# Kernel optimization log

Measured on AMD Instinct MI355X. Metric: run time of the kernel, lower is better.

## Reference

```python
import jax, jax.numpy as jnp
import numpy as np

RBF_DIM = 16
RBF_DMAX = 10.0
EPS = 1e-8


def _rbf(d):
    # GVP-style radial basis featurization: [..., RBF_DIM]
    mu = jnp.linspace(0.0, RBF_DMAX, RBF_DIM)
    sigma = RBF_DMAX / RBF_DIM
    return jnp.exp(-(((d[..., None] - mu) / sigma) ** 2))


def _norm_no_nan(x):
    return jnp.sqrt(jnp.clip(jnp.sum(x * x, axis=-1), EPS, None))


def setup_inputs() -> dict:
    key = jax.random.key(0)
    ks = jax.random.split(key, 16)
    N, Eu = 100000, 800000
    D_node, D_edge = 128, 64
    n_a, n_e = 16, 5
    s_t = jax.random.normal(ks[0], (N, D_node), jnp.float32)
    x_t = jax.random.normal(ks[1], (N, 3), jnp.float32) * 3.0
    v_t = jax.random.normal(ks[2], (N, 4, 3), jnp.float32)
    e_t = jax.random.normal(ks[3], (2 * Eu, D_edge), jnp.float32)
    dst_lig_x = x_t + jax.random.normal(ks[4], (N, 3), jnp.float32)
    dst_lig_a = jax.random.uniform(ks[5], (N, n_a), jnp.float32)
    dst_lig_e = jax.random.uniform(ks[6], (Eu, n_e), jnp.float32)
    # symmetric edge list: first Eu edges are "upper", second Eu their mirror
    src_u = jax.random.randint(ks[7], (Eu,), 0, N)
    dst_u = jax.random.randint(ks[8], (Eu,), 0, N)
    edge_src = jnp.concatenate([src_u, dst_u]).astype(jnp.int64)
    edge_dst = jnp.concatenate([dst_u, src_u]).astype(jnp.int64)
    # node residual MLP params (in = rbf + one-hot lig_a + s_t)
    din_n = RBF_DIM + n_a + D_node
    W1 = jax.random.normal(ks[9], (din_n, D_node), jnp.float32) / np.sqrt(din_n)
    b1 = jnp.zeros((D_node,), jnp.float32)
    W2 = jax.random.normal(ks[10], (D_node, D_node), jnp.float32) / np.sqrt(D_node)
    b2 = jnp.zeros((D_node,), jnp.float32)
    # edge residual MLP params (in = e_t + lig_e pred + rbf)
    din_e = D_edge + n_e + RBF_DIM
    We = jax.random.normal(ks[11], (din_e, D_edge), jnp.float32) / np.sqrt(din_e)
    be = jnp.zeros((D_edge,), jnp.float32)
    return {"s_t": s_t, "x_t": x_t, "v_t": v_t, "e_t": e_t,
            "dst_lig_x": dst_lig_x, "dst_lig_a": dst_lig_a, "dst_lig_e": dst_lig_e,
            "edge_src": edge_src, "edge_dst": edge_dst,
            "W1": W1, "b1": b1, "W2": W2, "b2": b2, "We": We, "be": be}


def reference(s_t, x_t, v_t, e_t, dst_lig_x, dst_lig_a, dst_lig_e,
              edge_src, edge_dst, W1, b1, W2, b2, We, be):
    # ---- node residual (lig_x generated -> RBF of |x_pred - x_t|; lig_a generated -> pred) ----
    x_diff = dst_lig_x - x_t                      # [N,3]
    dij = _norm_no_nan(x_diff)                    # [N]
    node_in = jnp.concatenate([_rbf(dij), dst_lig_a, s_t], axis=-1)
    h = jax.nn.silu(node_in @ W1 + b1)
    node_res = jax.nn.silu(h @ W2 + b2)
    node_out = s_t + node_res
    # overwrite last vector channel with unit displacement
    v_out = v_t.at[:, -1, :].set(x_diff / dij[:, None])
    # ---- lig_to_lig edge residual on upper edges, mirrored to lower edges ----
    Eu = edge_src.shape[0] // 2
    su, du = edge_src[:Eu], edge_dst[:Eu]
    d_t = _norm_no_nan(x_t[su] - x_t[du])         # current distances
    d_1 = _norm_no_nan(dst_lig_x[su] - dst_lig_x[du])  # predicted distances
    d_input = _rbf(d_1) - _rbf(d_t)               # [Eu, RBF_DIM]
    e_u = e_t[:Eu]
    edge_in = jnp.concatenate([e_u, dst_lig_e, d_input], axis=-1)
    edge_res = jax.nn.silu(edge_in @ We + be)
    feats = e_u + edge_res
    # original scatters feats into both upper-mask and ~upper-mask slots
    e_out = jnp.concatenate([feats, feats], axis=0)
    return node_out, v_out, e_out
```

## Files before the change

### kernel.cpp

```cpp
#include <hip/hip_runtime.h>
#include <math.h>

typedef short bf16x8 __attribute__((ext_vector_type(8)));
typedef float f32x4 __attribute__((ext_vector_type(4)));
typedef float fvec4 __attribute__((ext_vector_type(4)));

#define EBK 128

__device__ __forceinline__ float silu_f(float x) {
  return x / (1.0f + __expf(-x));
}
__device__ __forceinline__ unsigned short f2bf(float x) {
  union { float f; unsigned u; } v; v.f = x;
  unsigned r = v.u + 0x7FFFu + ((v.u >> 16) & 1u);
  return (unsigned short)(r >> 16);
}
__device__ __forceinline__ float bf2f(unsigned short h) {
  union { unsigned u; float f; } v; v.u = ((unsigned)h) << 16; return v.f;
}

__global__ __launch_bounds__(256)
void prep_kernel(const float* __restrict__ W1, const float* __restrict__ W2,
                 const float* __restrict__ We, unsigned short* __restrict__ ws)
{
  int i = blockIdx.x * 256 + threadIdx.x;
  if (i < 6144) {
    int col = i / 96, k = i - col * 96;
    float v = (k < 85) ? We[k * 64 + col] : 0.0f;
    ws[i] = f2bf(v);
  }
  int j = i - 6144;
  if (j >= 0 && j < 20480) {
    int col = j / 160, k = j - col * 160;
    ws[6144 + j] = f2bf(W1[k * 128 + col]);
  }
  int l = i - 26624;
  if (l >= 0 && l < 16384) {
    int col = l >> 7, k = l & 127;
    ws[26624 + l] = f2bf(W2[k * 128 + col]);
  }
}

__global__ __launch_bounds__(256, 4)
void node_kernel(const float* __restrict__ s_t,
                 const float* __restrict__ x_t,
                 const float* __restrict__ v_t,
                 const float* __restrict__ dst_lig_x,
                 const float* __restrict__ dst_lig_a,
                 const unsigned short* __restrict__ w1t, const float* __restrict__ b1,
                 const unsigned short* __restrict__ w2t, const float* __restrict__ b2,
                 float* __restrict__ node_out, float* __restrict__ v_out,
                 int N)
{
  __shared__ unsigned short A1[64][168];
  __shared__ unsigned short H [64][136];
  const int t = threadIdx.x;
  const int row0 = blockIdx.x * 64;
  const int w = t >> 6, lane = t & 63;

  #pragma unroll
  for (int p = 0; p < 8; ++p) {
    int i = p * 256 + t;
    int row = i >> 5, q = i & 31;
    if (row0 + row < N) {
      const fvec4 v = __builtin_nontemporal_load(
          reinterpret_cast<const fvec4*>(&s_t[(size_t)(row0 + row) * 128 + q * 4]));
      uint2 pk;
      pk.x = f2bf(v.x) | ((unsigned)f2bf(v.y) << 16);
      pk.y = f2bf(v.z) | ((unsigned)f2bf(v.w) << 16);
      *reinterpret_cast<uint2*>(&A1[row][32 + q * 4]) = pk;
    }
  }
  #pragma unroll
  for (int p = 0; p < 4; ++p) {
    int i = p * 256 + t;
    int el = i >> 4, m = i & 15;
    int row = row0 + el;
    if (row < N) {
      float dx = dst_lig_x[row*3+0] - x_t[row*3+0];
      float dy = dst_lig_x[row*3+1] - x_t[row*3+1];
      float dz = dst_lig_x[row*3+2] - x_t[row*3+2];
      float dij = sqrtf(fmaxf(dx*dx + dy*dy + dz*dz, 1e-8f));
      float tt = (dij - 0.66666667f * (float)m) * 1.6f;
      A1[el][m]      = f2bf(__expf(-tt * tt));
      A1[el][16 + m] = f2bf(dst_lig_a[(size_t)row * 16 + m]);
      if (m < 12) {
        float val;
        if (m < 9)       val = v_t[(size_t)row * 12 + m];
        else if (m == 9) val = dx / dij;
        else if (m == 10)val = dy / dij;
        else             val = dz / dij;
        __builtin_nontemporal_store(val, &v_out[(size_t)row * 12 + m]);
      }
    }
  }
  __syncthreads();

  const int mb = (w & 1) * 32;
  const int nb = (w >> 1) * 64;

  f32x4 acc[2][4] = {};
  #pragma unroll 1
  for (int ks = 0; ks < 5; ++ks) {
    const int ko = ks * 32 + ((lane >> 4) << 3);
    bf16x8 af[2], bfr[4];
    #pragma unroll
    for (int m = 0; m < 2; ++m)
      af[m] = *reinterpret_cast<const bf16x8*>(&A1[mb + m*16 + (lane & 15)][ko]);
    #pragma unroll
    for (int n = 0; n < 4; ++n)
      bfr[n] = *reinterpret_cast<const bf16x8*>(&w1t[(size_t)(nb + n*16 + (lane & 15)) * 160 + ko]);
    #pragma unroll
    for (int m = 0; m < 2; ++m)
      #pragma unroll
      for (int n = 0; n < 4; ++n)
        acc[m][n] = __builtin_amdgcn_mfma_f32_16x16x32_bf16(af[m], bfr[n], acc[m][n], 0, 0, 0);
  }
  #pragma unroll
  for (int n = 0; n < 4; ++n) {
    float bb = b1[nb + n*16 + (lane & 15)];
    #pragma unroll
    for (int m = 0; m < 2; ++m) {
      int r0 = mb + m*16 + ((lane >> 4) << 2);
      int c  = nb + n*16 + (lane & 15);
      #pragma unroll
      for (int r = 0; r < 4; ++r)
        H[r0 + r][c] = f2bf(silu_f(acc[m][n][r] + bb));
    }
  }
  __syncthreads();

  f32x4 acc2[2][4] = {};
  #pragma unroll 1
  for (int ks = 0; ks < 4; ++ks) {
    const int ko = ks * 32 + ((lane >> 4) << 3);
    bf16x8 af[2], bfr[4];
    #pragma unroll
    for (int m = 0; m < 2; ++m)
      af[m] = *reinterpret_cast<const bf16x8*>(&H[mb + m*16 + (lane & 15)][ko]);
    #pragma unroll
    for (int n = 0; n < 4; ++n)
      bfr[n] = *reinterpret_cast<const bf16x8*>(&w2t[(size_t)(nb + n*16 + (lane & 15)) * 128 + ko]);
    #pragma unroll
    for (int m = 0; m < 2; ++m)
      #pragma unroll
      for (int n = 0; n < 4; ++n)
        acc2[m][n] = __builtin_amdgcn_mfma_f32_16x16x32_bf16(af[m], bfr[n], acc2[m][n], 0, 0, 0);
  }
  #pragma unroll
  for (int n = 0; n < 4; ++n) {
    float bb = b2[nb + n*16 + (lane & 15)];
    #pragma unroll
    for (int m = 0; m < 2; ++m) {
      int r0 = mb + m*16 + ((lane >> 4) << 2);
      int c  = nb + n*16 + (lane & 15);
      #pragma unroll
      for (int r = 0; r < 4; ++r) {
        int row = row0 + r0 + r;
        if (row < N) {
          float o = bf2f(A1[r0 + r][32 + c]) + silu_f(acc2[m][n][r] + bb);
          __builtin_nontemporal_store(o, &node_out[(size_t)row * 128 + c]);
        }
      }
    }
  }
}

__global__ __launch_bounds__(256, 4)
void edge_kernel(const float* __restrict__ e_t,
                 const float* __restrict__ x_t,
                 const float* __restrict__ dst_lig_x,
                 const float* __restrict__ dst_lig_e,
                 const int* __restrict__ edge_src,
                 const int* __restrict__ edge_dst,
                 const unsigned short* __restrict__ wet, const float* __restrict__ be,
                 float* __restrict__ e_out0, float* __restrict__ e_out1,
                 int Eu)
{
  __shared__ unsigned short A[EBK][104];
  const int t = threadIdx.x;
  const int e0 = blockIdx.x * EBK;
  const int w = t >> 6, lane = t & 63;

  #pragma unroll
  for (int p = 0; p < 8; ++p) {
    int i = p * 256 + t;
    int row = i >> 4, cq = i & 15;
    if (e0 + row < Eu) {
      const fvec4 v = __builtin_nontemporal_load(
          reinterpret_cast<const fvec4*>(&e_t[(size_t)(e0 + row) * 64 + cq * 4]));
      uint2 pk;
      pk.x = f2bf(v.x) | ((unsigned)f2bf(v.y) << 16);
      pk.y = f2bf(v.z) | ((unsigned)f2bf(v.w) << 16);
      *reinterpret_cast<uint2*>(&A[row][cq * 4]) = pk;
    }
  }
  {
    const int el = t >> 1, which = t & 1;
    const int e = e0 + el;
    float dcur = 0.0f;
    if (e < Eu) {
      int su = edge_src[e], du = edge_dst[e];
      const float* base = which ? dst_lig_x : x_t;
      float u0 = base[su*3+0] - base[du*3+0];
      float u1 = base[su*3+1] - base[du*3+1];
      float u2 = base[su*3+2] - base[du*3+2];
      dcur = sqrtf(fmaxf(u0*u0 + u1*u1 + u2*u2, 1e-8f));
    }
    float doth = __shfl_xor(dcur, 1);
    float dt_ = which ? doth : dcur;
    float d1_ = which ? dcur : doth;
    if (e < Eu) {
      #pragma unroll
      for (int q = 0; q < 8; ++q) {
        int m = which * 8 + q;
        float mu = 0.66666667f * (float)m;
        float a1 = (d1_ - mu) * 1.6f, a2 = (dt_ - mu) * 1.6f;
        A[el][69 + m] = f2bf(__expf(-a1*a1) - __expf(-a2*a2));
      }
    }
  }
  #pragma unroll
  for (int q = 0; q < 3; ++q) {
    int i = q * 256 + t;
    if (i < EBK * 5) {
      int el = i / 5, c = i - el * 5;
      if (e0 + el < Eu) A[el][64 + c] = f2bf(dst_lig_e[(size_t)(e0 + el) * 5 + c]);
    }
  }
  #pragma unroll
  for (int q = 0; q < 6; ++q) {
    int i = q * 256 + t;
    if (i < EBK * 11) { int el = i / 11, c = i - el * 11; A[el][85 + c] = 0; }
  }
  __syncthreads();

  const int mb = w * 32;

  f32x4 acc[2][4] = {};
  #pragma unroll 1
  for (int ks = 0; ks < 3; ++ks) {
    const int ko = ks * 32 + ((lane >> 4) << 3);
    bf16x8 af[2], bfr[4];
    #pragma unroll
    for (int m = 0; m < 2; ++m)
      af[m] = *reinterpret_cast<const bf16x8*>(&A[mb + m*16 + (lane & 15)][ko]);
    #pragma unroll
    for (int n = 0; n < 4; ++n)
      bfr[n] = *reinterpret_cast<const bf16x8*>(&wet[(size_t)(n*16 + (lane & 15)) * 96 + ko]);
    #pragma unroll
    for (int m = 0; m < 2; ++m)
      #pragma unroll
      for (int n = 0; n < 4; ++n)
        acc[m][n] = __builtin_amdgcn_mfma_f32_16x16x32_bf16(af[m], bfr[n], acc[m][n], 0, 0, 0);
  }
  #pragma unroll
  for (int n = 0; n < 4; ++n) {
    float bb = be[n*16 + (lane & 15)];
    #pragma unroll
    for (int m = 0; m < 2; ++m) {
      int r0 = mb + m*16 + ((lane >> 4) << 2);
      int c  = n*16 + (lane & 15);
      #pragma unroll
      for (int r = 0; r < 4; ++r) {
        size_t eidx = (size_t)e0 + r0 + r;
        if ((int)eidx < Eu) {
          float feat = bf2f(A[r0 + r][c]) + silu_f(acc[m][n][r] + bb);
          __builtin_nontemporal_store(feat, &e_out0[eidx * 64 + c]);
          __builtin_nontemporal_store(feat, &e_out1[eidx * 64 + c]);
        }
      }
    }
  }
}

extern "C" void kernel_launch(void* const* d_in, const int* in_sizes, int n_in,
                              void* d_out, int out_size, void* d_ws, size_t ws_size,
                              hipStream_t stream) {
  const float* s_t       = (const float*)d_in[0];
  const float* x_t       = (const float*)d_in[1];
  const float* v_t       = (const float*)d_in[2];
  const float* e_t       = (const float*)d_in[3];
  const float* dst_lig_x = (const float*)d_in[4];
  const float* dst_lig_a = (const float*)d_in[5];
  const float* dst_lig_e = (const float*)d_in[6];
  const int*   edge_src  = (const int*)d_in[7];
  const int*   edge_dst  = (const int*)d_in[8];
  const float* W1        = (const float*)d_in[9];
  const float* b1        = (const float*)d_in[10];
  const float* W2        = (const float*)d_in[11];
  const float* b2        = (const float*)d_in[12];
  const float* We        = (const float*)d_in[13];
  const float* be        = (const float*)d_in[14];

  const int N  = in_sizes[0] / 128;
  const int Eu = in_sizes[3] / 128;

  float* out      = (float*)d_out;
  float* node_out = out;
  float* v_out    = out + (size_t)N * 128;
  float* e_out0   = v_out + (size_t)N * 12;
  float* e_out1   = e_out0 + (size_t)Eu * 64;

  unsigned short* wsp = (unsigned short*)d_ws;
  unsigned short* wet = wsp;
  unsigned short* w1t = wsp + 6144;
  unsigned short* w2t = wsp + 26624;

  prep_kernel<<<168, 256, 0, stream>>>(W1, W2, We, wsp);

  edge_kernel<<<(Eu + EBK - 1) / EBK, 256, 0, stream>>>(
      e_t, x_t, dst_lig_x, dst_lig_e, edge_src, edge_dst, wet, be,
      e_out0, e_out1, Eu);

  node_kernel<<<(N + 63) / 64, 256, 0, stream>>>(
      s_t, x_t, v_t, dst_lig_x, dst_lig_a, w1t, b1, w2t, b2,
      node_out, v_out, N);
}
```

Before: 255.7 us.

## Fuse node and edge kernels into one launch with interleaved block roles

Merges the separate edge and node kernels into a single kernel. Every fifth block does node work and the other blocks do edge work, with shared memory held in a union. This removes one launch and the tail bubble between the two kernels, and lets node and edge blocks run on the GPU at the same time. In exchange the shared memory per block becomes the larger of the two layouts and register use is the maximum of both paths, which could lower occupancy for edge blocks.

```diff
diff --git a/kernel.cpp b/kernel.cpp
--- a/kernel.cpp
+++ b/kernel.cpp
@@ -6,6 +6,7 @@
 typedef float fvec4 __attribute__((ext_vector_type(4)));
 
 #define EBK 128
+#define NBK 64
 
 __device__ __forceinline__ float silu_f(float x) {
   return x / (1.0f + __expf(-x));
@@ -41,233 +42,241 @@
   }
 }
 
+struct EdgeSmem { unsigned short A[EBK][104]; };
+struct NodeSmem { unsigned short A1[NBK][168]; unsigned short H[NBK][136]; };
+union FusedSmem { EdgeSmem e; NodeSmem n; };
+
 __global__ __launch_bounds__(256, 4)
-void node_kernel(const float* __restrict__ s_t,
-                 const float* __restrict__ x_t,
-                 const float* __restrict__ v_t,
-                 const float* __restrict__ dst_lig_x,
-                 const float* __restrict__ dst_lig_a,
-                 const unsigned short* __restrict__ w1t, const float* __restrict__ b1,
-                 const unsigned short* __restrict__ w2t, const float* __restrict__ b2,
-                 float* __restrict__ node_out, float* __restrict__ v_out,
-                 int N)
+void fused_kernel(const float* __restrict__ s_t,
+                  const float* __restrict__ x_t,
+                  const float* __restrict__ v_t,
+                  const float* __restrict__ e_t,
+                  const float* __restrict__ dst_lig_x,
+                  const float* __restrict__ dst_lig_a,
+                  const float* __restrict__ dst_lig_e,
+                  const int* __restrict__ edge_src,
+                  const int* __restrict__ edge_dst,
+                  const unsigned short* __restrict__ wsw,
+                  const float* __restrict__ b1, const float* __restrict__ b2,
+                  const float* __restrict__ be,
+                  float* __restrict__ node_out, float* __restrict__ v_out,
+                  float* __restrict__ e_out0, float* __restrict__ e_out1,
+                  int N, int Eu, int nNodeBlk, int nEdgeBlk)
 {
-  __shared__ unsigned short A1[64][168];
-  __shared__ unsigned short H [64][136];
+  __shared__ FusedSmem sm;
+  const int bid = blockIdx.x;
   const int t = threadIdx.x;
-  const int row0 = blockIdx.x * 64;
   const int w = t >> 6, lane = t & 63;
 
-  #pragma unroll
-  for (int p = 0; p < 8; ++p) {
-    int i = p * 256 + t;
-    int row = i >> 5, q = i & 31;
-    if (row0 + row < N) {
-      const fvec4 v = __builtin_nontemporal_load(
-          reinterpret_cast<const fvec4*>(&s_t[(size_t)(row0 + row) * 128 + q * 4]));
-      uint2 pk;
-      pk.x = f2bf(v.x) | ((unsigned)f2bf(v.y) << 16);
-      pk.y = f2bf(v.z) | ((unsigned)f2bf(v.w) << 16);
-      *reinterpret_cast<uint2*>(&A1[row][32 + q * 4]) = pk;
-    }
-  }
-  #pragma unroll
-  for (int p = 0; p < 4; ++p) {
-    int i = p * 256 + t;
-    int el = i >> 4, m = i & 15;
-    int row = row0 + el;
-    if (row < N) {
-      float dx = dst_lig_x[row*3+0] - x_t[row*3+0];
-      float dy = dst_lig_x[row*3+1] - x_t[row*3+1];
-      float dz = dst_lig_x[row*3+2] - x_t[row*3+2];
-      float dij = sqrtf(fmaxf(dx*dx + dy*dy + dz*dz, 1e-8f));
-      float tt = (dij - 0.66666667f * (float)m) * 1.6f;
-      A1[el][m]      = f2bf(__expf(-tt * tt));
-      A1[el][16 + m] = f2bf(dst_lig_a[(size_t)row * 16 + m]);
-      if (m < 12) {
-        float val;
-        if (m < 9)       val = v_t[(size_t)row * 12 + m];
-        else if (m == 9) val = dx / dij;
-        else if (m == 10)val = dy / dij;
-        else             val = dz / dij;
-        __builtin_nontemporal_store(val, &v_out[(size_t)row * 12 + m]);
-      }
-    }
-  }
-  __syncthreads();
-
-  const int mb = (w & 1) * 32;
-  const int nb = (w >> 1) * 64;
-
-  f32x4 acc[2][4] = {};
-  #pragma unroll 1
-  for (int ks = 0; ks < 5; ++ks) {
-    const int ko = ks * 32 + ((lane >> 4) << 3);
-    bf16x8 af[2], bfr[4];
-    #pragma unroll
-    for (int m = 0; m < 2; ++m)
-      af[m] = *reinterpret_cast<const bf16x8*>(&A1[mb + m*16 + (lane & 15)][ko]);
-    #pragma unroll
-    for (int n = 0; n < 4; ++n)
-      bfr[n] = *reinterpret_cast<const bf16x8*>(&w1t[(size_t)(nb + n*16 + (lane & 15)) * 160 + ko]);
-    #pragma unroll
-    for (int m = 0; m < 2; ++m)
+  if (bid % 5 == 4) {
+    const int nb = bid / 5;
+    if (nb >= nNodeBlk) return;
+    const int row0 = nb * NBK;
+    const unsigned short* w1t = wsw + 6144;
+    const unsigned short* w2t = wsw + 26624;
+    auto& A1 = sm.n.A1;
+    auto& H  = sm.n.H;
+
+    #pragma unroll
+    for (int p = 0; p < 8; ++p) {
+      int i = p * 256 + t;
+      int row = i >> 5, q = i & 31;
+      if (row0 + row < N) {
+        const fvec4 v = __builtin_nontemporal_load(
+            reinterpret_cast<const fvec4*>(&s_t[(size_t)(row0 + row) * 128 + q * 4]));
+        uint2 pk;
+        pk.x = f2bf(v.x) | ((unsigned)f2bf(v.y) << 16);
+        pk.y = f2bf(v.z) | ((unsigned)f2bf(v.w) << 16);
+        *reinterpret_cast<uint2*>(&A1[row][32 + q * 4]) = pk;
+      }
+    }
+    #pragma unroll
+    for (int p = 0; p < 4; ++p) {
+      int i = p * 256 + t;
+      int el = i >> 4, m = i & 15;
+      int row = row0 + el;
+      if (row < N) {
+        float dx = dst_lig_x[row*3+0] - x_t[row*3+0];
+        float dy = dst_lig_x[row*3+1] - x_t[row*3+1];
+        float dz = dst_lig_x[row*3+2] - x_t[row*3+2];
+        float dij = sqrtf(fmaxf(dx*dx + dy*dy + dz*dz, 1e-8f));
+        float tt = (dij - 0.66666667f * (float)m) * 1.6f;
+        A1[el][m]      = f2bf(__expf(-tt * tt));
+        A1[el][16 + m] = f2bf(dst_lig_a[(size_t)row * 16 + m]);
+        if (m < 12) {
+          float val;
+          if (m < 9)       val = v_t[(size_t)row * 12 + m];
+          else if (m == 9) val = dx / dij;
+          else if (m == 10)val = dy / dij;
+          else             val = dz / dij;
+          __builtin_nontemporal_store(val, &v_out[(size_t)row * 12 + m]);
+        }
+      }
+    }
+    __syncthreads();
+
+    const int mb = (w & 1) * 32;
+    const int nb2 = (w >> 1) * 64;
+
+    f32x4 acc[2][4] = {};
+    #pragma unroll 1
+    for (int ks = 0; ks < 5; ++ks) {
+      const int ko = ks * 32 + ((lane >> 4) << 3);
+      bf16x8 af[2], bfr[4];
+      #pragma unroll
+      for (int m = 0; m < 2; ++m)
+        af[m] = *reinterpret_cast<const bf16x8*>(&A1[mb + m*16 + (lane & 15)][ko]);
       #pragma unroll
       for (int n = 0; n < 4; ++n)
-        acc[m][n] = __builtin_amdgcn_mfma_f32_16x16x32_bf16(af[m], bfr[n], acc[m][n], 0, 0, 0);
-  }
-  #pragma unroll
-  for (int n = 0; n < 4; ++n) {
-    float bb = b1[nb + n*16 + (lane & 15)];
-    #pragma unroll
-    for (int m = 0; m < 2; ++m) {
-      int r0 = mb + m*16 + ((lane >> 4) << 2);
-      int c  = nb + n*16 + (lane & 15);
-      #pragma unroll
-      for (int r = 0; r < 4; ++r)
-        H[r0 + r][c] = f2bf(silu_f(acc[m][n][r] + bb));
-    }
-  }
-  __syncthreads();
-
-  f32x4 acc2[2][4] = {};
-  #pragma unroll 1
-  for (int ks = 0; ks < 4; ++ks) {
-    const int ko = ks * 32 + ((lane >> 4) << 3);
-    bf16x8 af[2], bfr[4];
-    #pragma unroll
-    for (int m = 0; m < 2; ++m)
-      af[m] = *reinterpret_cast<const bf16x8*>(&H[mb + m*16 + (lane & 15)][ko]);
-    #pragma unroll
-    for (int n = 0; n < 4; ++n)
-      bfr[n] = *reinterpret_cast<const bf16x8*>(&w2t[(size_t)(nb + n*16 + (lane & 15)) * 128 + ko]);
-    #pragma unroll
-    for (int m = 0; m < 2; ++m)
+        bfr[n] = *reinterpret_cast<const bf16x8*>(&w1t[(size_t)(nb2 + n*16 + (lane & 15)) * 160 + ko]);
+      #pragma unroll
+      for (int m = 0; m < 2; ++m)
+        #pragma unroll
+        for (int n = 0; n < 4; ++n)
+          acc[m][n] = __builtin_amdgcn_mfma_f32_16x16x32_bf16(af[m], bfr[n], acc[m][n], 0, 0, 0);
+    }
+    #pragma unroll
+    for (int n = 0; n < 4; ++n) {
+      float bb = b1[nb2 + n*16 + (lane & 15)];
+      #pragma unroll
+      for (int m = 0; m < 2; ++m) {
+        int r0 = mb + m*16 + ((lane >> 4) << 2);
+        int c  = nb2 + n*16 + (lane & 15);
+        #pragma unroll
+        for (int r = 0; r < 4; ++r)
+          H[r0 + r][c] = f2bf(silu_f(acc[m][n][r] + bb));
+      }
+    }
+    __syncthreads();
+
+    f32x4 acc2[2][4] = {};
+    #pragma unroll 1
+    for (int ks = 0; ks < 4; ++ks) {
+      const int ko = ks * 32 + ((lane >> 4) << 3);
+      bf16x8 af[2], bfr[4];
+      #pragma unroll
+      for (int m = 0; m < 2; ++m)
+        af[m] = *reinterpret_cast<const bf16x8*>(&H[mb + m*16 + (lane & 15)][ko]);
       #pragma unroll
       for (int n = 0; n < 4; ++n)
-        acc2[m][n] = __builtin_amdgcn_mfma_f32_16x16x32_bf16(af[m], bfr[n], acc2[m][n], 0, 0, 0);
-  }
-  #pragma unroll
-  for (int n = 0; n < 4; ++n) {
-    float bb = b2[nb + n*16 + (lane & 15)];
-    #pragma unroll
-    for (int m = 0; m < 2; ++m) {
-      int r0 = mb + m*16 + ((lane >> 4) << 2);
-      int c  = nb + n*16 + (lane & 15);
-      #pragma unroll
-      for (int r = 0; r < 4; ++r) {
-        int row = row0 + r0 + r;
-        if (row < N) {
-          float o = bf2f(A1[r0 + r][32 + c]) + silu_f(acc2[m][n][r] + bb);
-          __builtin_nontemporal_store(o, &node_out[(size_t)row * 128 + c]);
+        bfr[n] = *reinterpret_cast<const bf16x8*>(&w2t[(size_t)(nb2 + n*16 + (lane & 15)) * 128 + ko]);
+      #pragma unroll
+      for (int m = 0; m < 2; ++m)
+        #pragma unroll
+        for (int n = 0; n < 4; ++n)
+          acc2[m][n] = __builtin_amdgcn_mfma_f32_16x16x32_bf16(af[m], bfr[n], acc2[m][n], 0, 0, 0);
+    }
+    #pragma unroll
+    for (int n = 0; n < 4; ++n) {
+      float bb = b2[nb2 + n*16 + (lane & 15)];
+      #pragma unroll
+      for (int m = 0; m < 2; ++m) {
+        int r0 = mb + m*16 + ((lane >> 4) << 2);
+        int c  = nb2 + n*16 + (lane & 15);
+        #pragma unroll
+        for (int r = 0; r < 4; ++r) {
+          int row = row0 + r0 + r;
+          if (row < N) {
+            float o = bf2f(A1[r0 + r][32 + c]) + silu_f(acc2[m][n][r] + bb);
+            __builtin_nontemporal_store(o, &node_out[(size_t)row * 128 + c]);
+          }
         }
       }
     }
-  }
-}
-
-__global__ __launch_bounds__(256, 4)
-void edge_kernel(const float* __restrict__ e_t,
-                 const float* __restrict__ x_t,
-                 const float* __restrict__ dst_lig_x,
-                 const float* __restrict__ dst_lig_e,
-                 const int* __restrict__ edge_src,
-                 const int* __restrict__ edge_dst,
-                 const unsigned short* __restrict__ wet, const float* __restrict__ be,
-                 float* __restrict__ e_out0, float* __restrict__ e_out1,
-                 int Eu)
-{
-  __shared__ unsigned short A[EBK][104];
-  const int t = threadIdx.x;
-  const int e0 = blockIdx.x * EBK;
-  const int w = t >> 6, lane = t & 63;
-
-  #pragma unroll
-  for (int p = 0; p < 8; ++p) {
-    int i = p * 256 + t;
-    int row = i >> 4, cq = i & 15;
-    if (e0 + row < Eu) {
-      const fvec4 v = __builtin_nontemporal_load(
-          reinterpret_cast<const fvec4*>(&e_t[(size_t)(e0 + row) * 64 + cq * 4]));
-      uint2 pk;
-      pk.x = f2bf(v.x) | ((unsigned)f2bf(v.y) << 16);
-      pk.y = f2bf(v.z) | ((unsigned)f2bf(v.w) << 16);
-      *reinterpret_cast<uint2*>(&A[row][cq * 4]) = pk;
-    }
-  }
-  {
-    const int el = t >> 1, which = t & 1;
-    const int e = e0 + el;
-    float dcur = 0.0f;
-    if (e < Eu) {
-      int su = edge_src[e], du = edge_dst[e];
-      const float* base = which ? dst_lig_x : x_t;
-      float u0 = base[su*3+0] - base[du*3+0];
-      float u1 = base[su*3+1] - base[du*3+1];
-      float u2 = base[su*3+2] - base[du*3+2];
-      dcur = sqrtf(fmaxf(u0*u0 + u1*u1 + u2*u2, 1e-8f));
-    }
-    float doth = __shfl_xor(dcur, 1);
-    float dt_ = which ? doth : dcur;
-    float d1_ = which ? dcur : doth;
-    if (e < Eu) {
-      #pragma unroll
-      for (int q = 0; q < 8; ++q) {
-        int m = which * 8 + q;
-        float mu = 0.66666667f * (float)m;
-        float a1 = (d1_ - mu) * 1.6f, a2 = (dt_ - mu) * 1.6f;
-        A[el][69 + m] = f2bf(__expf(-a1*a1) - __expf(-a2*a2));
-      }
-    }
-  }
-  #pragma unroll
-  for (int q = 0; q < 3; ++q) {
-    int i = q * 256 + t;
-    if (i < EBK * 5) {
-      int el = i / 5, c = i - el * 5;
-      if (e0 + el < Eu) A[el][64 + c] = f2bf(dst_lig_e[(size_t)(e0 + el) * 5 + c]);
-    }
-  }
-  #pragma unroll
-  for (int q = 0; q < 6; ++q) {
-    int i = q * 256 + t;
-    if (i < EBK * 11) { int el = i / 11, c = i - el * 11; A[el][85 + c] = 0; }
-  }
-  __syncthreads();
-
-  const int mb = w * 32;
-
-  f32x4 acc[2][4] = {};
-  #pragma unroll 1
-  for (int ks = 0; ks < 3; ++ks) {
-    const int ko = ks * 32 + ((lane >> 4) << 3);
-    bf16x8 af[2], bfr[4];
-    #pragma unroll
-    for (int m = 0; m < 2; ++m)
-      af[m] = *reinterpret_cast<const bf16x8*>(&A[mb + m*16 + (lane & 15)][ko]);
-    #pragma unroll
-    for (int n = 0; n < 4; ++n)
-      bfr[n] = *reinterpret_cast<const bf16x8*>(&wet[(size_t)(n*16 + (lane & 15)) * 96 + ko]);
-    #pragma unroll
-    for (int m = 0; m < 2; ++m)
+  } else {
+    const int eb = bid - (bid + 1) / 5;
+    if (eb >= nEdgeBlk) return;
+    const int e0 = eb * EBK;
+    const unsigned short* wet = wsw;
+    auto& A = sm.e.A;
+
+    #pragma unroll
+    for (int p = 0; p < 8; ++p) {
+      int i = p * 256 + t;
+      int row = i >> 4, cq = i & 15;
+      if (e0 + row < Eu) {
+        const fvec4 v = __builtin_nontemporal_load(
+            reinterpret_cast<const fvec4*>(&e_t[(size_t)(e0 + row) * 64 + cq * 4]));
+        uint2 pk;
+        pk.x = f2bf(v.x) | ((unsigned)f2bf(v.y) << 16);
+        pk.y = f2bf(v.z) | ((unsigned)f2bf(v.w) << 16);
+        *reinterpret_cast<uint2*>(&A[row][cq * 4]) = pk;
+      }
+    }
+    {
+      const int el = t >> 1, which = t & 1;
+      const int e = e0 + el;
+      float dcur = 0.0f;
+      if (e < Eu) {
+        int su = edge_src[e], du = edge_dst[e];
+        const float* base = which ? dst_lig_x : x_t;
+        float u0 = base[su*3+0] - base[du*3+0];
+        float u1 = base[su*3+1] - base[du*3+1];
+        float u2 = base[su*3+2] - base[du*3+2];
+        dcur = sqrtf(fmaxf(u0*u0 + u1*u1 + u2*u2, 1e-8f));
+      }
+      float doth = __shfl_xor(dcur, 1);
+      float dt_ = which ? doth : dcur;
+      float d1_ = which ? dcur : doth;
+      if (e < Eu) {
+        #pragma unroll
+        for (int q = 0; q < 8; ++q) {
+          int m = which * 8 + q;
+          float mu = 0.66666667f * (float)m;
+          float a1 = (d1_ - mu) * 1.6f, a2 = (dt_ - mu) * 1.6f;
+          A[el][69 + m] = f2bf(__expf(-a1*a1) - __expf(-a2*a2));
+        }
+      }
+    }
+    #pragma unroll
+    for (int q = 0; q < 3; ++q) {
+      int i = q * 256 + t;
+      if (i < EBK * 5) {
+        int el = i / 5, c = i - el * 5;
+        if (e0 + el < Eu) A[el][64 + c] = f2bf(dst_lig_e[(size_t)(e0 + el) * 5 + c]);
+      }
+    }
+    #pragma unroll
+    for (int q = 0; q < 6; ++q) {
+      int i = q * 256 + t;
+      if (i < EBK * 11) { int el = i / 11, c = i - el * 11; A[el][85 + c] = 0; }
+    }
+    __syncthreads();
+
+    const int mb = w * 32;
+
+    f32x4 acc[2][4] = {};
+    #pragma unroll 1
+    for (int ks = 0; ks < 3; ++ks) {
+      const int ko = ks * 32 + ((lane >> 4) << 3);
+      bf16x8 af[2], bfr[4];
+      #pragma unroll
+      for (int m = 0; m < 2; ++m)
+        af[m] = *reinterpret_cast<const bf16x8*>(&A[mb + m*16 + (lane & 15)][ko]);
       #pragma unroll
       for (int n = 0; n < 4; ++n)
-        acc[m][n] = __builtin_amdgcn_mfma_f32_16x16x32_bf16(af[m], bfr[n], acc[m][n], 0, 0, 0);
-  }
-  #pragma unroll
-  for (int n = 0; n < 4; ++n) {
-    float bb = be[n*16 + (lane & 15)];
-    #pragma unroll
-    for (int m = 0; m < 2; ++m) {
-      int r0 = mb + m*16 + ((lane >> 4) << 2);
-      int c  = n*16 + (lane & 15);
-      #pragma unroll
-      for (int r = 0; r < 4; ++r) {
-        size_t eidx = (size_t)e0 + r0 + r;
-        if ((int)eidx < Eu) {
-          float feat = bf2f(A[r0 + r][c]) + silu_f(acc[m][n][r] + bb);
-          __builtin_nontemporal_store(feat, &e_out0[eidx * 64 + c]);
-          __builtin_nontemporal_store(feat, &e_out1[eidx * 64 + c]);
+        bfr[n] = *reinterpret_cast<const bf16x8*>(&wet[(size_t)(n*16 + (lane & 15)) * 96 + ko]);
+      #pragma unroll
+      for (int m = 0; m < 2; ++m)
+        #pragma unroll
+        for (int n = 0; n < 4; ++n)
+          acc[m][n] = __builtin_amdgcn_mfma_f32_16x16x32_bf16(af[m], bfr[n], acc[m][n], 0, 0, 0);
+    }
+    #pragma unroll
+    for (int n = 0; n < 4; ++n) {
+      float bb = be[n*16 + (lane & 15)];
+      #pragma unroll
+      for (int m = 0; m < 2; ++m) {
+        int r0 = mb + m*16 + ((lane >> 4) << 2);
+        int c  = n*16 + (lane & 15);
+        #pragma unroll
+        for (int r = 0; r < 4; ++r) {
+          size_t eidx = (size_t)e0 + r0 + r;
+          if ((int)eidx < Eu) {
+            float feat = bf2f(A[r0 + r][c]) + silu_f(acc[m][n][r] + bb);
+            __builtin_nontemporal_store(feat, &e_out0[eidx * 64 + c]);
+            __builtin_nontemporal_store(feat, &e_out1[eidx * 64 + c]);
+          }
         }
       }
     }
@@ -303,17 +312,15 @@
   float* e_out1   = e_out0 + (size_t)Eu * 64;
 
   unsigned short* wsp = (unsigned short*)d_ws;
-  unsigned short* wet = wsp;
-  unsigned short* w1t = wsp + 6144;
-  unsigned short* w2t = wsp + 26624;
+
+  const int NBLK = (N + NBK - 1) / NBK;
+  const int EBLK = (Eu + EBK - 1) / EBK;
+  int grid = 5 * NBLK;
+  if (4 * NBLK < EBLK) grid = 5 * NBLK + (EBLK - 4 * NBLK) + ((EBLK - 4 * NBLK) / 4 + 1);
 
   prep_kernel<<<168, 256, 0, stream>>>(W1, W2, We, wsp);
 
-  edge_kernel<<<(Eu + EBK - 1) / EBK, 256, 0, stream>>>(
-      e_t, x_t, dst_lig_x, dst_lig_e, edge_src, edge_dst, wet, be,
-      e_out0, e_out1, Eu);
-
-  node_kernel<<<(N + 63) / 64, 256, 0, stream>>>(
-      s_t, x_t, v_t, dst_lig_x, dst_lig_a, w1t, b1, w2t, b2,
-      node_out, v_out, N);
-}
+  fused_kernel<<<grid, 256, 0, stream>>>(
+      s_t, x_t, v_t, e_t, dst_lig_x, dst_lig_a, dst_lig_e, edge_src, edge_dst,
+      wsp, b1, b2, be, node_out, v_out, e_out0, e_out1, N, Eu, NBLK, EBLK);
+}
```

Measured after the change: 292.0 us. +14.2%, slower.

## Load edge features directly into MFMA fragments, shrink LDS, raise occupancy

Applied to the files above, without the earlier changes.

The edge kernel no longer stages e_t through shared memory. Each lane loads its fp32 e_t slice from global memory, converts it to bf16 in registers for the first two K-steps, and rereads e_t in fp32 for the residual add. Only the small lig_e/RBF tail stays in a much smaller shared tile, and the launch bound rises to 6 waves per SIMD. This removes LDS writes and reads for the bulk of the edge input and allows more occupancy, at the cost of uncoalesced row-strided global loads and a second read of e_t in the epilogue, which cache may absorb. The residual also now adds fp32 e_t instead of its bf16 copy.

```diff
diff --git a/kernel.cpp b/kernel.cpp
--- a/kernel.cpp
+++ b/kernel.cpp
@@ -6,6 +6,7 @@
 typedef float fvec4 __attribute__((ext_vector_type(4)));
 
 #define EBK 128
+#define NBK 64
 
 __device__ __forceinline__ float silu_f(float x) {
   return x / (1.0f + __expf(-x));
@@ -52,10 +53,10 @@
                  float* __restrict__ node_out, float* __restrict__ v_out,
                  int N)
 {
-  __shared__ unsigned short A1[64][168];
-  __shared__ unsigned short H [64][136];
+  __shared__ unsigned short A1[NBK][168];
+  __shared__ unsigned short H [NBK][136];
   const int t = threadIdx.x;
-  const int row0 = blockIdx.x * 64;
+  const int row0 = blockIdx.x * NBK;
   const int w = t >> 6, lane = t & 63;
 
   #pragma unroll
@@ -166,7 +167,7 @@
   }
 }
 
-__global__ __launch_bounds__(256, 4)
+__global__ __launch_bounds__(256, 6)
 void edge_kernel(const float* __restrict__ e_t,
                  const float* __restrict__ x_t,
                  const float* __restrict__ dst_lig_x,
@@ -177,24 +178,11 @@
                  float* __restrict__ e_out0, float* __restrict__ e_out1,
                  int Eu)
 {
-  __shared__ unsigned short A[EBK][104];
+  __shared__ unsigned short T[EBK][36];
   const int t = threadIdx.x;
   const int e0 = blockIdx.x * EBK;
   const int w = t >> 6, lane = t & 63;
 
-  #pragma unroll
-  for (int p = 0; p < 8; ++p) {
-    int i = p * 256 + t;
-    int row = i >> 4, cq = i & 15;
-    if (e0 + row < Eu) {
-      const fvec4 v = __builtin_nontemporal_load(
-          reinterpret_cast<const fvec4*>(&e_t[(size_t)(e0 + row) * 64 + cq * 4]));
-      uint2 pk;
-      pk.x = f2bf(v.x) | ((unsigned)f2bf(v.y) << 16);
-      pk.y = f2bf(v.z) | ((unsigned)f2bf(v.w) << 16);
-      *reinterpret_cast<uint2*>(&A[row][cq * 4]) = pk;
-    }
-  }
   {
     const int el = t >> 1, which = t & 1;
     const int e = e0 + el;
@@ -216,7 +204,7 @@
         int m = which * 8 + q;
         float mu = 0.66666667f * (float)m;
         float a1 = (d1_ - mu) * 1.6f, a2 = (dt_ - mu) * 1.6f;
-        A[el][69 + m] = f2bf(__expf(-a1*a1) - __expf(-a2*a2));
+        T[el][5 + m] = f2bf(__expf(-a1*a1) - __expf(-a2*a2));
       }
     }
   }
@@ -225,47 +213,74 @@
     int i = q * 256 + t;
     if (i < EBK * 5) {
       int el = i / 5, c = i - el * 5;
-      if (e0 + el < Eu) A[el][64 + c] = f2bf(dst_lig_e[(size_t)(e0 + el) * 5 + c]);
+      if (e0 + el < Eu) T[el][c] = f2bf(dst_lig_e[(size_t)(e0 + el) * 5 + c]);
     }
   }
   #pragma unroll
   for (int q = 0; q < 6; ++q) {
     int i = q * 256 + t;
-    if (i < EBK * 11) { int el = i / 11, c = i - el * 11; A[el][85 + c] = 0; }
+    if (i < EBK * 11) { int el = i / 11, c = i - el * 11; T[el][21 + c] = 0; }
   }
   __syncthreads();
 
   const int mb = w * 32;
+  const int lr = lane & 15;
+  const int koff = (lane >> 4) << 3;
 
   f32x4 acc[2][4] = {};
   #pragma unroll 1
-  for (int ks = 0; ks < 3; ++ks) {
-    const int ko = ks * 32 + ((lane >> 4) << 3);
+  for (int ks = 0; ks < 2; ++ks) {
     bf16x8 af[2], bfr[4];
     #pragma unroll
-    for (int m = 0; m < 2; ++m)
-      af[m] = *reinterpret_cast<const bf16x8*>(&A[mb + m*16 + (lane & 15)][ko]);
+    for (int m = 0; m < 2; ++m) {
+      int row = e0 + mb + m*16 + lr;
+      if (row >= Eu) row = Eu - 1;
+      const float* ap = &e_t[(size_t)row * 64 + ks * 32 + koff];
+      const fvec4 lo = *reinterpret_cast<const fvec4*>(ap);
+      const fvec4 hi = *reinterpret_cast<const fvec4*>(ap + 4);
+      union { bf16x8 v; unsigned u[4]; } pk;
+      pk.u[0] = f2bf(lo.x) | ((unsigned)f2bf(lo.y) << 16);
+      pk.u[1] = f2bf(lo.z) | ((unsigned)f2bf(lo.w) << 16);
+      pk.u[2] = f2bf(hi.x) | ((unsigned)f2bf(hi.y) << 16);
+      pk.u[3] = f2bf(hi.z) | ((unsigned)f2bf(hi.w) << 16);
+      af[m] = pk.v;
+    }
     #pragma unroll
     for (int n = 0; n < 4; ++n)
-      bfr[n] = *reinterpret_cast<const bf16x8*>(&wet[(size_t)(n*16 + (lane & 15)) * 96 + ko]);
+      bfr[n] = *reinterpret_cast<const bf16x8*>(&wet[(size_t)(n*16 + lr) * 96 + ks * 32 + koff]);
     #pragma unroll
     for (int m = 0; m < 2; ++m)
       #pragma unroll
       for (int n = 0; n < 4; ++n)
         acc[m][n] = __builtin_amdgcn_mfma_f32_16x16x32_bf16(af[m], bfr[n], acc[m][n], 0, 0, 0);
   }
+  {
+    bf16x8 af[2], bfr[4];
+    #pragma unroll
+    for (int m = 0; m < 2; ++m)
+      af[m] = *reinterpret_cast<const bf16x8*>(&T[mb + m*16 + lr][koff]);
+    #pragma unroll
+    for (int n = 0; n < 4; ++n)
+      bfr[n] = *reinterpret_cast<const bf16x8*>(&wet[(size_t)(n*16 + lr) * 96 + 64 + koff]);
+    #pragma unroll
+    for (int m = 0; m < 2; ++m)
+      #pragma unroll
+      for (int n = 0; n < 4; ++n)
+        acc[m][n] = __builtin_amdgcn_mfma_f32_16x16x32_bf16(af[m], bfr[n], acc[m][n], 0, 0, 0);
+  }
+
   #pragma unroll
   for (int n = 0; n < 4; ++n) {
-    float bb = be[n*16 + (lane & 15)];
+    float bb = be[n*16 + lr];
     #pragma unroll
     for (int m = 0; m < 2; ++m) {
       int r0 = mb + m*16 + ((lane >> 4) << 2);
-      int c  = n*16 + (lane & 15);
+      int c  = n*16 + lr;
       #pragma unroll
       for (int r = 0; r < 4; ++r) {
         size_t eidx = (size_t)e0 + r0 + r;
         if ((int)eidx < Eu) {
-          float feat = bf2f(A[r0 + r][c]) + silu_f(acc[m][n][r] + bb);
+          float feat = e_t[eidx * 64 + c] + silu_f(acc[m][n][r] + bb);
           __builtin_nontemporal_store(feat, &e_out0[eidx * 64 + c]);
           __builtin_nontemporal_store(feat, &e_out1[eidx * 64 + c]);
         }
@@ -313,7 +328,7 @@
       e_t, x_t, dst_lig_x, dst_lig_e, edge_src, edge_dst, wet, be,
       e_out0, e_out1, Eu);
 
-  node_kernel<<<(N + 63) / 64, 256, 0, stream>>>(
+  node_kernel<<<(N + NBK - 1) / NBK, 256, 0, stream>>>(
       s_t, x_t, v_t, dst_lig_x, dst_lig_a, w1t, b1, w2t, b2,
       node_out, v_out, N);
 }
```

Result: faster. 246.9 us, median of 3 (-3.4%).
